# Optimization experiments

Hardware: AMD Instinct MI355X
Metric: run time of the kernel (lower is better)

The kernel has to match this reference:

```python
import jax, jax.numpy as jnp
import numpy as np

N_NODES = 50000
N_EDGES = 400000
NODE_DIM = 128
NUM_BASIS = 20
MUL0, MUL1, MUL2 = 128, 64, 32          # 128x0e + 64x1e + 32x2e
NUM_IRREPS = MUL0 + MUL1 + MUL2         # 224
SPH_DIM = MUL0 + 3 * MUL1 + 5 * MUL2    # 480
HIDDEN = NODE_DIM + NUM_IRREPS          # 352
EPS = 1e-5


def layer_norm(x, g, b):
    mu = x.mean(-1, keepdims=True)
    var = ((x - mu) ** 2).mean(-1, keepdims=True)
    return (x - mu) * jax.lax.rsqrt(var + EPS) * g + b


def o3_layer_norm(x, w, b):
    # Equivariant layer norm per irrep block (Equiformer-style, component normalization).
    s = x[:, :MUL0]                                    # l=0 scalars [N,128]
    v = x[:, MUL0:MUL0 + 3 * MUL1].reshape(-1, MUL1, 3)  # l=1 [N,64,3]
    t = x[:, MUL0 + 3 * MUL1:].reshape(-1, MUL2, 5)      # l=2 [N,32,5]
    s = s - s.mean(-1, keepdims=True)
    s = s * jax.lax.rsqrt((s ** 2).mean(-1, keepdims=True) + EPS) * w[:MUL0] + b
    nv = (v ** 2).mean(axis=(-1, -2))[:, None, None]
    v = v * jax.lax.rsqrt(nv + EPS) * w[MUL0:MUL0 + MUL1][None, :, None]
    nt = (t ** 2).mean(axis=(-1, -2))[:, None, None]
    t = t * jax.lax.rsqrt(nt + EPS) * w[MUL0 + MUL1:][None, :, None]
    return jnp.concatenate([s, v.reshape(-1, 3 * MUL1), t.reshape(-1, 5 * MUL2)], axis=-1)


def sph_harm(vec):
    # e3nn spherical harmonics (normalize=True, normalization='component') up to l=2.
    u = vec * jax.lax.rsqrt((vec ** 2).sum(-1, keepdims=True))
    x, y, z = u[:, 0], u[:, 1], u[:, 2]
    s15 = np.float32(np.sqrt(15.0))
    s5 = np.float32(np.sqrt(5.0))
    sh1 = np.float32(np.sqrt(3.0)) * u  # [E,3]
    sh2 = jnp.stack([s15 * x * z,
                     s15 * x * y,
                     s5 * (y * y - 0.5 * (x * x + z * z)),
                     s15 * y * z,
                     0.5 * s15 * (z * z - x * x)], axis=-1)  # [E,5]
    return sh1, sh2


def _forward(x_scalar, x_spherical, rbf, vec, W1, b1, W2, b2, Wrbf, ln_g, ln_b, o3_w, o3_b, edge_index):
    dst, src = edge_index[0], edge_index[1]
    scalar_in = layer_norm(x_scalar, ln_g, ln_b)          # [N,128]
    spherical_in = o3_layer_norm(x_spherical, o3_w, o3_b)  # [N,480]
    h = jax.nn.silu(scalar_in @ W1 + b1)
    scalar_out = h @ W2 + b2                               # [N,352]
    filter_weight = rbf @ Wrbf                             # [E,352]
    filter_out = scalar_out[src] * filter_weight           # gather + elementwise [E,352]
    gate = filter_out[:, :NUM_IRREPS]                      # [E,224]
    message_scalar = filter_out[:, NUM_IRREPS:]            # [E,128]
    sh1, sh2 = sph_harm(vec)
    g0 = gate[:, :MUL0]
    g1 = gate[:, MUL0:MUL0 + MUL1]
    g2 = gate[:, MUL0 + MUL1:]
    # ElementwiseTensorProduct(edge_irreps, '224x0e'): scalar gate per irrep; l=0 SH == 1.
    msg1 = (g1[:, :, None] * sh1[:, None, :]).reshape(-1, 3 * MUL1)
    msg2 = (g2[:, :, None] * sh2[:, None, :]).reshape(-1, 5 * MUL2)
    message_spherical = jnp.concatenate([g0, msg1, msg2], axis=-1)  # [E,480]
    new_scalar = scalar_in.at[dst].add(message_scalar)
    new_spherical = spherical_in.at[dst].add(message_spherical)
    return new_scalar, new_spherical


def setup_inputs() -> dict:
    key = jax.random.key(0)
    ks = jax.random.split(key, 8)
    return {
        "x_scalar": jax.random.normal(ks[0], (N_NODES, NODE_DIM), dtype=jnp.float32),
        "x_spherical": jax.random.normal(ks[1], (N_NODES, SPH_DIM), dtype=jnp.float32),
        "rbf": jax.random.normal(ks[2], (N_EDGES, NUM_BASIS), dtype=jnp.float32),
        "vec": jax.random.normal(ks[3], (N_EDGES, 3), dtype=jnp.float32),
        "W1": jax.random.normal(ks[4], (NODE_DIM, NODE_DIM), dtype=jnp.float32) * 0.05,
        "b1": jnp.zeros((NODE_DIM,), jnp.float32),
        "W2": jax.random.normal(ks[5], (NODE_DIM, HIDDEN), dtype=jnp.float32) * 0.05,
        "b2": jnp.zeros((HIDDEN,), jnp.float32),
        "Wrbf": jax.random.normal(ks[6], (NUM_BASIS, HIDDEN), dtype=jnp.float32) * 0.05,
        "ln_g": jnp.ones((NODE_DIM,), jnp.float32),
        "ln_b": jnp.zeros((NODE_DIM,), jnp.float32),
        "o3_w": jnp.ones((NUM_IRREPS,), jnp.float32),
        "o3_b": jnp.zeros((MUL0,), jnp.float32),
        "edge_index": jax.random.randint(ks[7], (2, N_EDGES), 0, N_NODES),
    }


def reference(x_scalar, x_spherical, rbf, vec, W1, b1, W2, b2, Wrbf, ln_g, ln_b, o3_w, o3_b, edge_index):
    return _forward(x_scalar, x_spherical, rbf, vec, W1, b1, W2, b2, Wrbf, ln_g, ln_b, o3_w, o3_b, edge_index)
```

## Files before the change

### kernel.cpp

```cpp
#include <hip/hip_runtime.h>
#include <hip/hip_bf16.h>

#define N_DIM   128
#define MUL0    128
#define MUL1    64
#define MUL2    32
#define NIRR    224
#define SPHD    480
#define HID     352
#define NBASIS  20
#define EPSV    1e-5f

typedef __attribute__((ext_vector_type(8))) short bf16x8;
typedef __attribute__((ext_vector_type(4))) float f32x4;

__device__ __forceinline__ float wave_sum(float v) {
  #pragma unroll
  for (int o = 32; o > 0; o >>= 1) v += __shfl_xor(v, o, 64);
  return v;
}

__device__ __forceinline__ unsigned short f2bf(float f) {
  unsigned int u = __float_as_uint(f);
  u = (u + 0x7fff + ((u >> 16) & 1)) >> 16;
  return (unsigned short)u;
}

__device__ __forceinline__ float bf2f(unsigned short v) {
  return __uint_as_float(((unsigned int)v) << 16);
}

__global__ __launch_bounds__(256) void node_norm_kernel(
    const float* __restrict__ x_scalar, const float* __restrict__ x_sph,
    const float* __restrict__ ln_g, const float* __restrict__ ln_b,
    const float* __restrict__ o3_w, const float* __restrict__ o3_b,
    float* __restrict__ out_scal, float* __restrict__ out_sph, int n_nodes) {
  const int n = blockIdx.x * 4 + (threadIdx.x >> 6);
  if (n >= n_nodes) return;
  const int l = threadIdx.x & 63;

  const float* xs = x_scalar + (size_t)n * N_DIM;
  float a0 = xs[l], a1 = xs[l + 64];
  float mu = wave_sum(a0 + a1) * (1.f / 128.f);
  float d0 = a0 - mu, d1 = a1 - mu;
  float var = wave_sum(d0 * d0 + d1 * d1) * (1.f / 128.f);
  float sc = rsqrtf(var + EPSV);
  float* os = out_scal + (size_t)n * N_DIM;
  os[l]      = d0 * sc * ln_g[l]      + ln_b[l];
  os[l + 64] = d1 * sc * ln_g[l + 64] + ln_b[l + 64];

  const float* xp = x_sph + (size_t)n * SPHD;
  float s0 = xp[l], s1 = xp[l + 64];
  mu = wave_sum(s0 + s1) * (1.f / 128.f);
  d0 = s0 - mu; d1 = s1 - mu;
  var = wave_sum(d0 * d0 + d1 * d1) * (1.f / 128.f);
  sc = rsqrtf(var + EPSV);
  float* op = out_sph + (size_t)n * SPHD;
  op[l]      = d0 * sc * o3_w[l]      + o3_b[l];
  op[l + 64] = d1 * sc * o3_w[l + 64] + o3_b[l + 64];

  float v0 = xp[128 + l], v1 = xp[128 + 64 + l], v2 = xp[128 + 128 + l];
  float nv = wave_sum(v0 * v0 + v1 * v1 + v2 * v2) * (1.f / 192.f);
  sc = rsqrtf(nv + EPSV);
  op[128 + l]       = v0 * sc * o3_w[MUL0 + (l) / 3];
  op[128 + 64 + l]  = v1 * sc * o3_w[MUL0 + (l + 64) / 3];
  op[128 + 128 + l] = v2 * sc * o3_w[MUL0 + (l + 128) / 3];

  float t0 = xp[320 + l], t1 = xp[320 + 64 + l];
  float t2 = (l < 32) ? xp[320 + 128 + l] : 0.f;
  float nt = wave_sum(t0 * t0 + t1 * t1 + t2 * t2) * (1.f / 160.f);
  sc = rsqrtf(nt + EPSV);
  op[320 + l]      = t0 * sc * o3_w[MUL0 + MUL1 + (l) / 5];
  op[320 + 64 + l] = t1 * sc * o3_w[MUL0 + MUL1 + (l + 64) / 5];
  if (l < 32) op[320 + 128 + l] = t2 * sc * o3_w[MUL0 + MUL1 + (l + 128) / 5];
}

__global__ void pack_b_kernel(const float* __restrict__ B, unsigned short* __restrict__ Bp,
                              int N, int NT) {
  int id = blockIdx.x * 256 + threadIdx.x;
  int total = 4 * NT * 64;
  if (id >= total) return;
  int lane = id & 63;
  int tmp = id >> 6;
  int nt = tmp % NT, ks = tmp / NT;
  int n = nt * 16 + (lane & 15);
  int kb = ks * 32 + (lane >> 4) * 8;
  unsigned short* o = Bp + (size_t)id * 8;
  #pragma unroll
  for (int j = 0; j < 8; ++j)
    o[j] = (n < N) ? f2bf(B[(size_t)(kb + j) * N + n]) : (unsigned short)0;
}

__global__ void pack_wt_kernel(const float* __restrict__ Wrbf, float* __restrict__ Wt) {
  int id = blockIdx.x * 256 + threadIdx.x;
  if (id >= HID * NBASIS) return;
  int c = id / NBASIS, k = id - c * NBASIS;
  Wt[id] = Wrbf[k * HID + c];
}

template <bool A_BF16, bool SILU, bool OUT_BF16, bool PERM>
__global__ __launch_bounds__(256) void mfma_gemm_kernel(
    const void* __restrict__ Ap, const unsigned short* __restrict__ Bp,
    const float* __restrict__ bias, void* __restrict__ Cp,
    int M, int N, int NT) {
  const int lane = threadIdx.x & 63;
  const int wave = threadIdx.x >> 6;
  const int bm = blockIdx.x * 64 + wave * 16;
  const int bn = blockIdx.y * 64;
  const int q = lane >> 4;
  const int arow = min(bm + (lane & 15), M - 1);

  f32x4 acc[4] = {};
  #pragma unroll
  for (int ks = 0; ks < 4; ++ks) {
    const int k = ks * 32 + q * 8;
    bf16x8 a;
    if (A_BF16) {
      a = *(const bf16x8*)((const unsigned short*)Ap + (size_t)arow * 128 + k);
    } else {
      const float* ap = (const float*)Ap + (size_t)arow * 128 + k;
      float4 f0 = *(const float4*)ap;
      float4 f1 = *(const float4*)(ap + 4);
      union { bf16x8 v; unsigned short s[8]; } cv;
      cv.s[0] = f2bf(f0.x); cv.s[1] = f2bf(f0.y); cv.s[2] = f2bf(f0.z); cv.s[3] = f2bf(f0.w);
      cv.s[4] = f2bf(f1.x); cv.s[5] = f2bf(f1.y); cv.s[6] = f2bf(f1.z); cv.s[7] = f2bf(f1.w);
      a = cv.v;
    }
    #pragma unroll
    for (int nt = 0; nt < 4; ++nt) {
      bf16x8 b = *(const bf16x8*)(Bp + ((size_t)(ks * NT + blockIdx.y * 4 + nt) * 64 + lane) * 8);
      acc[nt] = __builtin_amdgcn_mfma_f32_16x16x32_bf16(a, b, acc[nt], 0, 0, 0);
    }
  }
  #pragma unroll
  for (int nt = 0; nt < 4; ++nt) {
    int col = bn + nt * 16 + (lane & 15);
    if (col >= N) continue;
    float bz = bias[col];
    int pcol = col;
    if (PERM) pcol = (col < 96) ? (2 * col) : ((col < 256) ? (col + 96) : (2 * (col - 256) + 1));
    #pragma unroll
    for (int i = 0; i < 4; ++i) {
      int r = bm + q * 4 + i;
      if (r >= M) continue;
      float v = acc[nt][i] + bz;
      if (SILU) v = v / (1.f + __expf(-v));
      if (OUT_BF16) ((unsigned short*)Cp)[(size_t)r * N + pcol] = f2bf(v);
      else          ((float*)Cp)[(size_t)r * N + pcol] = v;
    }
  }
}

__global__ void hist_kernel(const int* __restrict__ ei, int* __restrict__ deg, int n_edges) {
  int e = blockIdx.x * blockDim.x + threadIdx.x;
  if (e < n_edges) atomicAdd(&deg[ei[e]], 1);
}

__global__ __launch_bounds__(1024) void scan_part_kernel(
    const int* __restrict__ deg, int* __restrict__ offs, int* __restrict__ bsum, int n) {
  __shared__ int wsum[16];
  const int tid = threadIdx.x, lane = tid & 63, wid = tid >> 6;
  int i = blockIdx.x * 1024 + tid;
  int v = (i < n) ? deg[i] : 0;
  int s = v;
  #pragma unroll
  for (int o = 1; o < 64; o <<= 1) {
    int t = __shfl_up(s, o, 64);
    if (lane >= o) s += t;
  }
  if (lane == 63) wsum[wid] = s;
  __syncthreads();
  if (wid == 0) {
    int ws = (lane < 16) ? wsum[lane] : 0;
    #pragma unroll
    for (int o = 1; o < 16; o <<= 1) {
      int t = __shfl_up(ws, o, 64);
      if (lane >= o) ws += t;
    }
    if (lane < 16) wsum[lane] = ws;
  }
  __syncthreads();
  int excl = ((wid == 0) ? 0 : wsum[wid - 1]) + s - v;
  if (i < n) offs[i] = excl;
  if (tid == 1023) bsum[blockIdx.x] = wsum[15];
}

__global__ __launch_bounds__(64) void scan_tops_kernel(
    const int* __restrict__ bsum, int* __restrict__ bbase, int* __restrict__ offs,
    int nb, int n) {
  const int lane = threadIdx.x;
  int v = (lane < nb) ? bsum[lane] : 0;
  int s = v;
  #pragma unroll
  for (int o = 1; o < 64; o <<= 1) {
    int t = __shfl_up(s, o, 64);
    if (lane >= o) s += t;
  }
  if (lane < nb) bbase[lane] = s - v;
  if (lane == 63) offs[n] = s;
}

__global__ __launch_bounds__(1024) void scan_add_kernel(
    int* __restrict__ offs, const int* __restrict__ bbase, int n) {
  int i = blockIdx.x * 1024 + threadIdx.x;
  if (i < n) offs[i] += bbase[blockIdx.x];
}

__global__ void fill_kernel(const int* __restrict__ ei, const int* __restrict__ offs,
                            int* __restrict__ cursor, const int* __restrict__ edge_src,
                            const float* __restrict__ rbf, const float* __restrict__ vec,
                            float* __restrict__ rbf_s, float* __restrict__ vec_s,
                            int* __restrict__ src_s, int n_edges) {
  int e = blockIdx.x * blockDim.x + threadIdx.x;
  if (e < n_edges) {
    int d = ei[e];
    int p = atomicAdd(&cursor[d], 1);
    int ii = offs[d] + p;
    src_s[ii] = edge_src[e];
    const float4* rp = (const float4*)(rbf + (size_t)e * NBASIS);
    float4* op = (float4*)(rbf_s + (size_t)ii * NBASIS);
    op[0] = rp[0]; op[1] = rp[1]; op[2] = rp[2]; op[3] = rp[3]; op[4] = rp[4];
    vec_s[(size_t)ii * 3]     = vec[(size_t)e * 3];
    vec_s[(size_t)ii * 3 + 1] = vec[(size_t)e * 3 + 1];
    vec_s[(size_t)ii * 3 + 2] = vec[(size_t)e * 3 + 2];
  }
}

#define NPB 4
#define CHUNK 64
#define S3f  1.7320508075688772f
#define S15f 3.872983346207417f
#define S5f  2.2360679774997896f

__device__ __forceinline__ void so_load(const unsigned short* __restrict__ so,
                                        int src, int t, bool hasB,
                                        float& sA, float& sB) {
  const unsigned short* p = so + (size_t)src * HID;
  if (hasB) {
    unsigned int u = *(const unsigned int*)(p + 2 * t);
    sA = __uint_as_float(u << 16);
    sB = __uint_as_float(u & 0xffff0000u);
  } else {
    sA = bf2f(p[t + 96]);
    sB = 0.f;
  }
}

__global__ __launch_bounds__(256, 4) void gather_kernel(
    const float* __restrict__ rbf_s, const float* __restrict__ vec_s,
    const float* __restrict__ Wt, const unsigned short* __restrict__ so,
    const int* __restrict__ src_s, const int* __restrict__ offs,
    float* __restrict__ out_scal, float* __restrict__ out_sph, int n_nodes) {
  __shared__ float rbf_l[CHUNK * NBASIS];
  __shared__ float sh_l[CHUNK * 8];
  __shared__ int   src_l[CHUNK];

  const int t = threadIdx.x;
  const bool hasB = (t < 96);

  const f32x4* wap = (const f32x4*)(Wt + (size_t)t * NBASIS);
  f32x4 wA0 = wap[0], wA1 = wap[1], wA2 = wap[2], wA3 = wap[3], wA4 = wap[4];
  const f32x4* wbp = (const f32x4*)(Wt + (size_t)(hasB ? (256 + t) : 256) * NBASIS);
  f32x4 wB0 = wbp[0], wB1 = wbp[1], wB2 = wbp[2], wB3 = wbp[3], wB4 = wbp[4];
  asm volatile("" : "+v"(wA0), "+v"(wA1), "+v"(wA2), "+v"(wA3), "+v"(wA4));
  asm volatile("" : "+v"(wB0), "+v"(wB1), "+v"(wB2), "+v"(wB3), "+v"(wB4));

  const int n0 = blockIdx.x * NPB;
  if (n0 >= n_nodes) return;
  const int nE = min(n0 + NPB, n_nodes);
  const int E0 = offs[n0], E1 = offs[nE];

  int eb0[NPB], eb1[NPB];
  #pragma unroll
  for (int i = 0; i < NPB; ++i) {
    int nd = n0 + i;
    eb0[i] = (nd < n_nodes) ? offs[nd] : E1;
    eb1[i] = (nd < n_nodes) ? offs[nd + 1] : E1;
  }

  float a0[NPB] = {}, a1[NPB] = {}, a2[NPB] = {}, a3[NPB] = {}, a4[NPB] = {}, aB[NPB] = {};

  for (int C0 = E0; C0 < E1; C0 += CHUNK) {
    const int C1 = min(C0 + CHUNK, E1);
    const int ns = C1 - C0;

    for (int i = t; i < ns * NBASIS; i += 256)
      rbf_l[i] = rbf_s[(size_t)C0 * NBASIS + i];
    if (t < ns) {
      const int ii = C0 + t;
      src_l[t] = src_s[ii];
      float vx = vec_s[3 * (size_t)ii], vy = vec_s[3 * (size_t)ii + 1], vz = vec_s[3 * (size_t)ii + 2];
      float rn = rsqrtf(vx * vx + vy * vy + vz * vz);
      float x = vx * rn, y = vy * rn, z = vz * rn;
      float* sp = &sh_l[t * 8];
      sp[0] = S3f * x; sp[1] = S3f * y; sp[2] = S3f * z;
      sp[3] = S15f * x * z;
      sp[4] = S15f * x * y;
      sp[5] = S5f * (y * y - 0.5f * (x * x + z * z));
      sp[6] = S15f * y * z;
      sp[7] = 0.5f * S15f * (z * z - x * x);
    }
    __syncthreads();

    auto edge = [&](int il, float sA, float sB, int nn) {
      const float* rbp = &rbf_l[il * NBASIS];
      f32x4 r0 = *(const f32x4*)(rbp);
      f32x4 r1 = *(const f32x4*)(rbp + 4);
      f32x4 r2 = *(const f32x4*)(rbp + 8);
      f32x4 r3 = *(const f32x4*)(rbp + 12);
      f32x4 r4 = *(const f32x4*)(rbp + 16);
      float fwA = 0.f;
      fwA += r0[0] * wA0[0]; fwA += r0[1] * wA0[1]; fwA += r0[2] * wA0[2]; fwA += r0[3] * wA0[3];
      fwA += r1[0] * wA1[0]; fwA += r1[1] * wA1[1]; fwA += r1[2] * wA1[2]; fwA += r1[3] * wA1[3];
      fwA += r2[0] * wA2[0]; fwA += r2[1] * wA2[1]; fwA += r2[2] * wA2[2]; fwA += r2[3] * wA2[3];
      fwA += r3[0] * wA3[0]; fwA += r3[1] * wA3[1]; fwA += r3[2] * wA3[2]; fwA += r3[3] * wA3[3];
      fwA += r4[0] * wA4[0]; fwA += r4[1] * wA4[1]; fwA += r4[2] * wA4[2]; fwA += r4[3] * wA4[3];
      float fA = sA * fwA;

      if (t < 128) {
        a0[nn] += fA;
      } else if (t < 224) {
        const float* sp = &sh_l[il * 8];
        if (t < 192) {
          a0[nn] += fA * sp[0]; a1[nn] += fA * sp[1]; a2[nn] += fA * sp[2];
        } else {
          a0[nn] += fA * sp[3]; a1[nn] += fA * sp[4]; a2[nn] += fA * sp[5];
          a3[nn] += fA * sp[6]; a4[nn] += fA * sp[7];
        }
      } else {
        a0[nn] += fA;
      }

      if (hasB) {
        float fwB = 0.f;
        fwB += r0[0] * wB0[0]; fwB += r0[1] * wB0[1]; fwB += r0[2] * wB0[2]; fwB += r0[3] * wB0[3];
        fwB += r1[0] * wB1[0]; fwB += r1[1] * wB1[1]; fwB += r1[2] * wB1[2]; fwB += r1[3] * wB1[3];
        fwB += r2[0] * wB2[0]; fwB += r2[1] * wB2[1]; fwB += r2[2] * wB2[2]; fwB += r2[3] * wB2[3];
        fwB += r3[0] * wB3[0]; fwB += r3[1] * wB3[1]; fwB += r3[2] * wB3[2]; fwB += r3[3] * wB3[3];
        fwB += r4[0] * wB4[0]; fwB += r4[1] * wB4[1]; fwB += r4[2] * wB4[2]; fwB += r4[3] * wB4[3];
        aB[nn] += sB * fwB;
      }
    };

    #pragma unroll
    for (int nn = 0; nn < NPB; ++nn) {
      const int lo = max(eb0[nn], C0);
      const int hi = min(eb1[nn], C1);
      int ii = lo;
      for (; ii + 2 <= hi; ii += 2) {
        const int il0 = ii - C0, il1 = il0 + 1;
        const int s0 = src_l[il0], s1 = src_l[il1];
        float sA0, sB0, sA1, sB1;
        so_load(so, s0, t, hasB, sA0, sB0);
        so_load(so, s1, t, hasB, sA1, sB1);
        edge(il0, sA0, sB0, nn);
        edge(il1, sA1, sB1, nn);
      }
      if (ii < hi) {
        const int il0 = ii - C0;
        const int s0 = src_l[il0];
        float sA0, sB0;
        so_load(so, s0, t, hasB, sA0, sB0);
        edge(il0, sA0, sB0, nn);
      }
    }
    __syncthreads();
  }

  #pragma unroll
  for (int nn = 0; nn < NPB; ++nn) {
    const int node = n0 + nn;
    if (node >= n_nodes) break;
    float* sph = out_sph + (size_t)node * SPHD;
    float* scl = out_scal + (size_t)node * N_DIM;
    if (t < 128) {
      sph[t] += a0[nn];
    } else if (t < 192) {
      float* p = sph + 128 + 3 * (t - 128);
      p[0] += a0[nn]; p[1] += a1[nn]; p[2] += a2[nn];
    } else if (t < 224) {
      float* p = sph + 320 + 5 * (t - 192);
      p[0] += a0[nn]; p[1] += a1[nn]; p[2] += a2[nn]; p[3] += a3[nn]; p[4] += a4[nn];
    } else {
      scl[t - 224] += a0[nn];
    }
    if (hasB) scl[t + 32] += aB[nn];
  }
}

extern "C" void kernel_launch(void* const* d_in, const int* in_sizes, int n_in,
                              void* d_out, int out_size, void* d_ws, size_t ws_size,
                              hipStream_t stream) {
  const float* x_scalar = (const float*)d_in[0];
  const float* x_sph    = (const float*)d_in[1];
  const float* rbf      = (const float*)d_in[2];
  const float* vec      = (const float*)d_in[3];
  const float* W1       = (const float*)d_in[4];
  const float* b1       = (const float*)d_in[5];
  const float* W2       = (const float*)d_in[6];
  const float* b2       = (const float*)d_in[7];
  const float* Wrbf     = (const float*)d_in[8];
  const float* ln_g     = (const float*)d_in[9];
  const float* ln_b     = (const float*)d_in[10];
  const float* o3_w     = (const float*)d_in[11];
  const float* o3_b     = (const float*)d_in[12];
  const int*   edge_idx = (const int*)d_in[13];

  const int n_nodes = in_sizes[0] / N_DIM;
  const int n_edges = in_sizes[2] / NBASIS;

  float* out_scal = (float*)d_out;
  float* out_sph  = out_scal + (size_t)n_nodes * N_DIM;

  float* rbf_s = (float*)d_ws;
  float* vec_s = rbf_s + (size_t)n_edges * NBASIS;
  int*   src_s = (int*)(vec_s + (size_t)n_edges * 3);
  unsigned short* so_bf = (unsigned short*)(src_s + n_edges);
  unsigned short* h_bf  = so_bf + (size_t)n_nodes * HID;
  unsigned short* bp1   = h_bf + (size_t)n_nodes * N_DIM;
  unsigned short* bp2   = bp1 + 16384;
  int* deg    = (int*)(bp2 + 49152);
  int* cursor = deg + n_nodes;
  int* offs   = cursor + n_nodes;
  int* bsum   = offs + n_nodes + 1;
  int* bbase  = bsum + 64;
  float* Wt   = (float*)(bbase + 64);

  const int* edge_dst = edge_idx;
  const int* edge_src = edge_idx + n_edges;

  node_norm_kernel<<<(n_nodes + 3) / 4, 256, 0, stream>>>(
      x_scalar, x_sph, ln_g, ln_b, o3_w, o3_b, out_scal, out_sph, n_nodes);

  pack_b_kernel<<<8, 256, 0, stream>>>(W1, bp1, N_DIM, 8);
  pack_b_kernel<<<24, 256, 0, stream>>>(W2, bp2, HID, 24);
  pack_wt_kernel<<<(HID * NBASIS + 255) / 256, 256, 0, stream>>>(Wrbf, Wt);

  {
    dim3 g((n_nodes + 63) / 64, 2);
    mfma_gemm_kernel<false, true, true, false><<<g, 256, 0, stream>>>(
        out_scal, bp1, b1, h_bf, n_nodes, N_DIM, 8);
  }
  {
    dim3 g((n_nodes + 63) / 64, 6);
    mfma_gemm_kernel<true, false, true, true><<<g, 256, 0, stream>>>(
        h_bf, bp2, b2, so_bf, n_nodes, HID, 24);
  }

  hipMemsetAsync(deg, 0, sizeof(int) * 2 * n_nodes, stream);
  hist_kernel<<<(n_edges + 255) / 256, 256, 0, stream>>>(edge_dst, deg, n_edges);
  const int nb = (n_nodes + 1023) / 1024;
  scan_part_kernel<<<nb, 1024, 0, stream>>>(deg, offs, bsum, n_nodes);
  scan_tops_kernel<<<1, 64, 0, stream>>>(bsum, bbase, offs, nb, n_nodes);
  scan_add_kernel<<<nb, 1024, 0, stream>>>(offs, bbase, n_nodes);
  fill_kernel<<<(n_edges + 255) / 256, 256, 0, stream>>>(
      edge_dst, offs, cursor, edge_src, rbf, vec, rbf_s, vec_s, src_s, n_edges);

  gather_kernel<<<(n_nodes + NPB - 1) / NPB, 256, 0, stream>>>(
      rbf_s, vec_s, Wt, so_bf, src_s, offs, out_scal, out_sph, n_nodes);
}
```

Baseline: 698.7 us.

## Compute per-edge filter weights with bf16 MFMA into shared memory in gather

```diff
diff --git a/kernel.cpp b/kernel.cpp
--- a/kernel.cpp
+++ b/kernel.cpp
@@ -28,6 +28,12 @@
 
 __device__ __forceinline__ float bf2f(unsigned short v) {
   return __uint_as_float(((unsigned int)v) << 16);
+}
+
+__device__ __forceinline__ unsigned int cvt_pk_bf16(float a, float b) {
+  unsigned int r;
+  asm("v_cvt_pk_bf16_f32 %0, %1, %2" : "=v"(r) : "v"(a), "v"(b));
+  return r;
 }
 
 __global__ __launch_bounds__(256) void node_norm_kernel(
@@ -91,11 +97,18 @@
     o[j] = (n < N) ? f2bf(B[(size_t)(kb + j) * N + n]) : (unsigned short)0;
 }
 
-__global__ void pack_wt_kernel(const float* __restrict__ Wrbf, float* __restrict__ Wt) {
+__global__ void pack_bw_kernel(const float* __restrict__ Wrbf, unsigned short* __restrict__ Bpw) {
   int id = blockIdx.x * 256 + threadIdx.x;
-  if (id >= HID * NBASIS) return;
-  int c = id / NBASIS, k = id - c * NBASIS;
-  Wt[id] = Wrbf[k * HID + c];
+  if (id >= 22 * 64) return;
+  int lane = id & 63, nt = id >> 6;
+  int n = nt * 16 + (lane & 15);
+  int kb = (lane >> 4) * 8;
+  unsigned short* o = Bpw + (size_t)id * 8;
+  #pragma unroll
+  for (int j = 0; j < 8; ++j) {
+    int k = kb + j;
+    o[j] = (k < NBASIS) ? f2bf(Wrbf[(size_t)k * HID + n]) : (unsigned short)0;
+  }
 }
 
 template <bool A_BF16, bool SILU, bool OUT_BF16, bool PERM>
@@ -226,8 +239,9 @@
   }
 }
 
-#define NPB 4
-#define CHUNK 64
+#define NPB 3
+#define CHUNK 32
+#define FWPAD 36
 #define S3f  1.7320508075688772f
 #define S15f 3.872983346207417f
 #define S5f  2.2360679774997896f
@@ -246,24 +260,19 @@
   }
 }
 
-__global__ __launch_bounds__(256, 4) void gather_kernel(
+__global__ __launch_bounds__(256) void gather_kernel(
     const float* __restrict__ rbf_s, const float* __restrict__ vec_s,
-    const float* __restrict__ Wt, const unsigned short* __restrict__ so,
+    const unsigned short* __restrict__ Bpw, const unsigned short* __restrict__ so,
     const int* __restrict__ src_s, const int* __restrict__ offs,
     float* __restrict__ out_scal, float* __restrict__ out_sph, int n_nodes) {
   __shared__ float rbf_l[CHUNK * NBASIS];
   __shared__ float sh_l[CHUNK * 8];
   __shared__ int   src_l[CHUNK];
+  __shared__ unsigned short fw_l[HID * FWPAD];
 
   const int t = threadIdx.x;
+  const int lane = t & 63, w = t >> 6, q = lane >> 4;
   const bool hasB = (t < 96);
-
-  const f32x4* wap = (const f32x4*)(Wt + (size_t)t * NBASIS);
-  f32x4 wA0 = wap[0], wA1 = wap[1], wA2 = wap[2], wA3 = wap[3], wA4 = wap[4];
-  const f32x4* wbp = (const f32x4*)(Wt + (size_t)(hasB ? (256 + t) : 256) * NBASIS);
-  f32x4 wB0 = wbp[0], wB1 = wbp[1], wB2 = wbp[2], wB3 = wbp[3], wB4 = wbp[4];
-  asm volatile("" : "+v"(wA0), "+v"(wA1), "+v"(wA2), "+v"(wA3), "+v"(wA4));
-  asm volatile("" : "+v"(wB0), "+v"(wB1), "+v"(wB2), "+v"(wB3), "+v"(wB4));
 
   const int n0 = blockIdx.x * NPB;
   if (n0 >= n_nodes) return;
@@ -302,21 +311,40 @@
     }
     __syncthreads();
 
-    auto edge = [&](int il, float sA, float sB, int nn) {
-      const float* rbp = &rbf_l[il * NBASIS];
-      f32x4 r0 = *(const f32x4*)(rbp);
-      f32x4 r1 = *(const f32x4*)(rbp + 4);
-      f32x4 r2 = *(const f32x4*)(rbp + 8);
-      f32x4 r3 = *(const f32x4*)(rbp + 12);
-      f32x4 r4 = *(const f32x4*)(rbp + 16);
-      float fwA = 0.f;
-      fwA += r0[0] * wA0[0]; fwA += r0[1] * wA0[1]; fwA += r0[2] * wA0[2]; fwA += r0[3] * wA0[3];
-      fwA += r1[0] * wA1[0]; fwA += r1[1] * wA1[1]; fwA += r1[2] * wA1[2]; fwA += r1[3] * wA1[3];
-      fwA += r2[0] * wA2[0]; fwA += r2[1] * wA2[1]; fwA += r2[2] * wA2[2]; fwA += r2[3] * wA2[3];
-      fwA += r3[0] * wA3[0]; fwA += r3[1] * wA3[1]; fwA += r3[2] * wA3[2]; fwA += r3[3] * wA3[3];
-      fwA += r4[0] * wA4[0]; fwA += r4[1] * wA4[1]; fwA += r4[2] * wA4[2]; fwA += r4[3] * wA4[3];
+    {
+      const int et = w >> 1;
+      const int ntb = (w & 1) * 11;
+      const int mrow = et * 16 + (lane & 15);
+      const float* ar = &rbf_l[mrow * NBASIS];
+      f32x4 lo = {}, hi = {};
+      if (q < 2) {
+        lo = *(const f32x4*)(ar + q * 8);
+        hi = *(const f32x4*)(ar + q * 8 + 4);
+      } else if (q == 2) {
+        lo = *(const f32x4*)(ar + 16);
+      }
+      union { bf16x8 v; unsigned int u[4]; } af;
+      af.u[0] = cvt_pk_bf16(lo[0], lo[1]);
+      af.u[1] = cvt_pk_bf16(lo[2], lo[3]);
+      af.u[2] = cvt_pk_bf16(hi[0], hi[1]);
+      af.u[3] = cvt_pk_bf16(hi[2], hi[3]);
+      #pragma unroll
+      for (int j = 0; j < 11; ++j) {
+        const int nt = ntb + j;
+        bf16x8 b = *(const bf16x8*)(Bpw + (size_t)(nt * 64 + lane) * 8);
+        f32x4 acc = {};
+        acc = __builtin_amdgcn_mfma_f32_16x16x32_bf16(af.v, b, acc, 0, 0, 0);
+        const int col = nt * 16 + (lane & 15);
+        uint2 pk;
+        pk.x = cvt_pk_bf16(acc[0], acc[1]);
+        pk.y = cvt_pk_bf16(acc[2], acc[3]);
+        *(uint2*)&fw_l[col * FWPAD + et * 16 + q * 4] = pk;
+      }
+    }
+    __syncthreads();
+
+    auto edge = [&](int il, float sA, float sB, float fwA, float fwB, int nn) {
       float fA = sA * fwA;
-
       if (t < 128) {
         a0[nn] += fA;
       } else if (t < 224) {
@@ -330,16 +358,7 @@
       } else {
         a0[nn] += fA;
       }
-
-      if (hasB) {
-        float fwB = 0.f;
-        fwB += r0[0] * wB0[0]; fwB += r0[1] * wB0[1]; fwB += r0[2] * wB0[2]; fwB += r0[3] * wB0[3];
-        fwB += r1[0] * wB1[0]; fwB += r1[1] * wB1[1]; fwB += r1[2] * wB1[2]; fwB += r1[3] * wB1[3];
-        fwB += r2[0] * wB2[0]; fwB += r2[1] * wB2[1]; fwB += r2[2] * wB2[2]; fwB += r2[3] * wB2[3];
-        fwB += r3[0] * wB3[0]; fwB += r3[1] * wB3[1]; fwB += r3[2] * wB3[2]; fwB += r3[3] * wB3[3];
-        fwB += r4[0] * wB4[0]; fwB += r4[1] * wB4[1]; fwB += r4[2] * wB4[2]; fwB += r4[3] * wB4[3];
-        aB[nn] += sB * fwB;
-      }
+      if (hasB) aB[nn] += sB * fwB;
     };
 
     #pragma unroll
@@ -353,15 +372,24 @@
         float sA0, sB0, sA1, sB1;
         so_load(so, s0, t, hasB, sA0, sB0);
         so_load(so, s1, t, hasB, sA1, sB1);
-        edge(il0, sA0, sB0, nn);
-        edge(il1, sA1, sB1, nn);
+        float fwA0 = bf2f(fw_l[t * FWPAD + il0]);
+        float fwA1 = bf2f(fw_l[t * FWPAD + il1]);
+        float fwB0 = 0.f, fwB1 = 0.f;
+        if (hasB) {
+          fwB0 = bf2f(fw_l[(256 + t) * FWPAD + il0]);
+          fwB1 = bf2f(fw_l[(256 + t) * FWPAD + il1]);
+        }
+        edge(il0, sA0, sB0, fwA0, fwB0, nn);
+        edge(il1, sA1, sB1, fwA1, fwB1, nn);
       }
       if (ii < hi) {
         const int il0 = ii - C0;
         const int s0 = src_l[il0];
         float sA0, sB0;
         so_load(so, s0, t, hasB, sA0, sB0);
-        edge(il0, sA0, sB0, nn);
+        float fwA0 = bf2f(fw_l[t * FWPAD + il0]);
+        float fwB0 = hasB ? bf2f(fw_l[(256 + t) * FWPAD + il0]) : 0.f;
+        edge(il0, sA0, sB0, fwA0, fwB0, nn);
       }
     }
     __syncthreads();
@@ -419,12 +447,12 @@
   unsigned short* h_bf  = so_bf + (size_t)n_nodes * HID;
   unsigned short* bp1   = h_bf + (size_t)n_nodes * N_DIM;
   unsigned short* bp2   = bp1 + 16384;
-  int* deg    = (int*)(bp2 + 49152);
+  unsigned short* bpw   = bp2 + 49152;
+  int* deg    = (int*)(bpw + 11264);
   int* cursor = deg + n_nodes;
   int* offs   = cursor + n_nodes;
   int* bsum   = offs + n_nodes + 1;
   int* bbase  = bsum + 64;
-  float* Wt   = (float*)(bbase + 64);
 
   const int* edge_dst = edge_idx;
   const int* edge_src = edge_idx + n_edges;
@@ -434,7 +462,7 @@
 
   pack_b_kernel<<<8, 256, 0, stream>>>(W1, bp1, N_DIM, 8);
   pack_b_kernel<<<24, 256, 0, stream>>>(W2, bp2, HID, 24);
-  pack_wt_kernel<<<(HID * NBASIS + 255) / 256, 256, 0, stream>>>(Wrbf, Wt);
+  pack_bw_kernel<<<6, 256, 0, stream>>>(Wrbf, bpw);
 
   {
     dim3 g((n_nodes + 63) / 64, 2);
@@ -457,5 +485,5 @@
       edge_dst, offs, cursor, edge_src, rbf, vec, rbf_s, vec_s, src_s, n_edges);
 
   gather_kernel<<<(n_nodes + NPB - 1) / NPB, 256, 0, stream>>>(
-      rbf_s, vec_s, Wt, so_bf, src_s, offs, out_scal, out_sph, n_nodes);
-}
+      rbf_s, vec_s, bpw, so_bf, src_s, offs, out_scal, out_sph, n_nodes);
+}
```

Result: faster. 642.3 us (-8.1%).
